# Optimization experiments

Measured on AMD Instinct MI355X. Metric: run time of the kernel, lower is better.

## Reference

```python
import jax, jax.numpy as jnp
import numpy as np

N = 100000      # num nodes
E = 500000      # num edges
IN_DIM = 128
OUT_DIM = 128
H = 8           # n_heads
DK = OUT_DIM // H  # 16


def setup_inputs() -> dict:
    key = jax.random.key(0)
    ks = jax.random.split(key, 16)
    s = 1.0 / np.sqrt(IN_DIM)
    inp = {
        "x": jax.random.normal(ks[0], (N, IN_DIM), dtype=jnp.float32),
        "edge_index": jax.random.randint(ks[1], (2, E), 0, N, dtype=jnp.int64),
        # per-type linear layers (num_types=1)
        "Wk": jax.random.uniform(ks[2], (OUT_DIM, IN_DIM), jnp.float32, -s, s),
        "bk": jnp.zeros((OUT_DIM,), jnp.float32),
        "Wq": jax.random.uniform(ks[3], (OUT_DIM, IN_DIM), jnp.float32, -s, s),
        "bq": jnp.zeros((OUT_DIM,), jnp.float32),
        "Wv": jax.random.uniform(ks[4], (OUT_DIM, IN_DIM), jnp.float32, -s, s),
        "bv": jnp.zeros((OUT_DIM,), jnp.float32),
        "Wa": jax.random.uniform(ks[5], (OUT_DIM, OUT_DIM), jnp.float32, -s, s),
        "ba": jnp.zeros((OUT_DIM,), jnp.float32),
        # per-relation params (num_relations=1), xavier-uniform for d_k x d_k mats
        "R_att": jax.random.uniform(ks[6], (H, DK, DK), jnp.float32, -np.sqrt(6.0 / (2 * DK)), np.sqrt(6.0 / (2 * DK))),
        "R_msg": jax.random.uniform(ks[7], (H, DK, DK), jnp.float32, -np.sqrt(6.0 / (2 * DK)), np.sqrt(6.0 / (2 * DK))),
        "R_pri": jnp.ones((H,), jnp.float32),
        "skip": jnp.ones((), jnp.float32),
    }
    return inp


def reference(x, edge_index, Wk, bk, Wq, bq, Wv, bv, Wa, ba, R_att, R_msg, R_pri, skip):
    sqrt_dk = jnp.asarray(np.sqrt(DK), x.dtype)
    # per-node projections -> [N, H, DK]
    k = (x @ Wk.T + bk).reshape(N, H, DK)
    q = (x @ Wq.T + bq).reshape(N, H, DK)
    v = (x @ Wv.T + bv).reshape(N, H, DK)
    src, dst = edge_index[0], edge_index[1]
    # edge gather: [E, H, DK]
    ke = jnp.einsum('ehd,hdf->ehf', k[src], R_att)
    ve = jnp.einsum('ehd,hdf->ehf', v[src], R_msg)
    qe = q[dst]
    # attention scores [E, H]; softmax over the edge axis (as in the original)
    att = jnp.sum(qe * ke, axis=-1) * R_pri / sqrt_dk
    att = jax.nn.softmax(att, axis=0)
    # weighted sum over all edges -> [H, DK] -> [OUT_DIM]
    out = jnp.einsum('eh,ehf->hf', att, ve).reshape(-1)
    out = Wa @ out + ba  # a_linear on the pooled vector
    alpha = jax.nn.sigmoid(skip)
    # broadcast skip mix against node inputs -> [N, OUT_DIM]
    return out * alpha + x * (1.0 - alpha)
```

## Files before the change

kernel.cpp:

```cpp
#include <hip/hip_runtime.h>
#include <hip/hip_bf16.h>

#define NN 100000
#define EE 500000
#define NB2 256
#define EGRID 2048

typedef __attribute__((ext_vector_type(8))) __bf16 bf16x8;
typedef __attribute__((ext_vector_type(4))) float f32x4;
typedef __attribute__((ext_vector_type(2))) float f32x2;

static const long long OFF_KQ8  = 0;
static const long long OFF_VB   = 6400000;
static const long long OFF_WGT  = 12800000;
static const long long OFF_PART = 13600000;
static const long long OFF_OUTV = 13634816;
static const long long OFF_CNT  = 13634944;
static const long long OFF_WF   = 13635008;
static const long long OFF_BALL = 13659584;

__device__ inline unsigned short f2bf(float f) {
    unsigned int u = __float_as_uint(f);
    unsigned int r = (u + 0x7FFFu + ((u >> 16) & 1u)) >> 16;
    return (unsigned short)r;
}
__device__ inline unsigned int pack2bf(float a, float b) {
    return (unsigned int)f2bf(a) | ((unsigned int)f2bf(b) << 16);
}
#define LOF(u) __uint_as_float((u) << 16)
#define HIF(u) __uint_as_float((u) & 0xffff0000u)

#if __has_builtin(__builtin_amdgcn_cvt_pk_fp8_f32) && __has_builtin(__builtin_amdgcn_cvt_pk_f32_fp8)
#define HW_FP8 1
#endif

__device__ inline unsigned char enc_fp8(float f) {
#ifdef HW_FP8
    int p = __builtin_amdgcn_cvt_pk_fp8_f32(f, f, 0, false);
    return (unsigned char)(p & 0xff);
#else
    unsigned int u = __float_as_uint(f);
    unsigned int s = (u >> 24) & 0x80u;
    unsigned int a = u & 0x7fffffffu;
    if (a >= 0x43e80000u) return (unsigned char)(s | 0x7e);
    if (a < 0x3c800000u) {
        float av = __uint_as_float(a);
        unsigned int m = (unsigned int)rintf(av * 512.0f);
        return (unsigned char)(s | m);
    }
    unsigned int base = a - 0x3c000000u;
    unsigned int r = (base + 0x7ffffu + ((base >> 20) & 1u)) >> 20;
    return (unsigned char)(s | r);
#endif
}

#ifndef HW_FP8
__device__ inline float dec1_fp8(unsigned int b) {
    unsigned int s = (b & 0x80u) << 24;
    unsigned int em = b & 0x7fu;
    float v;
    if (em >= 8u) v = __uint_as_float(s | ((em + 960u) << 20));
    else {
        v = (float)em * 0.001953125f;
        v = __uint_as_float(__float_as_uint(v) | s);
    }
    return v;
}
#endif

__device__ inline float dot4_fp8(unsigned int ka, unsigned int qa, float d) {
#ifdef HW_FP8
    f32x2 k0 = __builtin_amdgcn_cvt_pk_f32_fp8((int)ka, false);
    f32x2 k1 = __builtin_amdgcn_cvt_pk_f32_fp8((int)ka, true);
    f32x2 q0 = __builtin_amdgcn_cvt_pk_f32_fp8((int)qa, false);
    f32x2 q1 = __builtin_amdgcn_cvt_pk_f32_fp8((int)qa, true);
    d = fmaf(k0.x, q0.x, d); d = fmaf(k0.y, q0.y, d);
    d = fmaf(k1.x, q1.x, d); d = fmaf(k1.y, q1.y, d);
    return d;
#else
    #pragma unroll
    for (int i = 0; i < 4; ++i)
        d = fmaf(dec1_fp8((ka >> (8*i)) & 0xff), dec1_fp8((qa >> (8*i)) & 0xff), d);
    return d;
#endif
}

__global__ void prep(const float* __restrict__ Wk, const float* __restrict__ bk,
                     const float* __restrict__ Wq, const float* __restrict__ bq,
                     const float* __restrict__ Wv, const float* __restrict__ bv,
                     const float* __restrict__ R_att,
                     unsigned short* __restrict__ Wf, float* __restrict__ ball,
                     float* __restrict__ Wgt, unsigned int* __restrict__ counter) {
    int j = blockIdx.x;
    int c = threadIdx.x;
    float w;
    if (j < 128) {
        w = Wk[j * 128 + c];
        if (c == 0) ball[j] = bk[j];
    } else if (j < 256) {
        int h = (j - 128) >> 4, d = (j - 128) & 15;
        const float* Rrow = R_att + h * 256 + d * 16;
        float s = 0.f;
        #pragma unroll
        for (int f = 0; f < 16; ++f)
            s = fmaf(Rrow[f], Wq[(h * 16 + f) * 128 + c], s);
        w = s;
        if (c == 0) {
            float sb = 0.f;
            for (int f = 0; f < 16; ++f)
                sb = fmaf(Rrow[f], bq[h * 16 + f], sb);
            ball[j] = sb;
        }
    } else {
        w = Wv[(j - 256) * 128 + c];
        if (c == 0) ball[j] = bv[j - 256];
    }
    int g = j >> 7, wc = (j >> 6) & 1, n = (j >> 4) & 3, lr = j & 15;
    int kk = c >> 5, lk = (c >> 3) & 3, i = c & 7;
    int idx = ((((g * 2 + wc) * 4 + n) * 4 + kk) * 64 + lk * 16 + lr) * 8 + i;
    Wf[idx] = f2bf(w);
    for (int z = j * 128 + c; z < 200000; z += 384 * 128)
        ((float4*)Wgt)[z] = make_float4(0.f, 0.f, 0.f, 0.f);
    if (j == 0 && c == 0) *counter = 0u;
}

__global__ __launch_bounds__(256) void proj_mfma(const float* __restrict__ x,
                                                 const unsigned short* __restrict__ Wf,
                                                 const float* __restrict__ ball,
                                                 unsigned char* __restrict__ kq8,
                                                 unsigned char* __restrict__ vb) {
    __shared__ __align__(16) char cs[16384];
    int tid = threadIdx.x;
    int lane = tid & 63, wv = tid >> 6, wr = wv >> 1, wc = wv & 1;
    int lrow = lane & 15, lk = lane >> 4;
    long long row0 = (long long)blockIdx.x * 64;
    int g = blockIdx.y;
    int col0 = g * 128;

    const float* xr[2];
    #pragma unroll
    for (int m = 0; m < 2; ++m) {
        long long gr = row0 + wr * 32 + m * 16 + lrow;
        if (gr >= NN) gr = NN - 1;
        xr[m] = x + gr * 128;
    }
    const unsigned short* bfb = Wf + (size_t)((g * 2 + wc) * 16) * 512 + lane * 8;

    f32x4 acc[2][4];
    #pragma unroll
    for (int m = 0; m < 2; ++m)
        #pragma unroll
        for (int n = 0; n < 4; ++n)
            acc[m][n] = f32x4{0.f, 0.f, 0.f, 0.f};

    #pragma unroll
    for (int kk = 0; kk < 4; ++kk) {
        bf16x8 a[2], b[4];
        #pragma unroll
        for (int m = 0; m < 2; ++m) {
            const float4* p = (const float4*)(xr[m] + (kk * 4 + lk) * 8);
            float4 u0 = p[0], u1 = p[1];
            union { uint4 u; bf16x8 v; } cv;
            cv.u.x = pack2bf(u0.x, u0.y); cv.u.y = pack2bf(u0.z, u0.w);
            cv.u.z = pack2bf(u1.x, u1.y); cv.u.w = pack2bf(u1.z, u1.w);
            a[m] = cv.v;
        }
        #pragma unroll
        for (int n = 0; n < 4; ++n)
            b[n] = *(const bf16x8*)(bfb + (size_t)(n * 4 + kk) * 512);
        #pragma unroll
        for (int m = 0; m < 2; ++m)
            #pragma unroll
            for (int n = 0; n < 4; ++n)
                acc[m][n] = __builtin_amdgcn_mfma_f32_16x16x32_bf16(a[m], b[n], acc[m][n], 0, 0, 0);
    }

    float bias[4];
    #pragma unroll
    for (int n = 0; n < 4; ++n) bias[n] = ball[col0 + wc * 64 + n * 16 + lrow];

    if (g < 2) {
        unsigned char* C = (unsigned char*)cs;
        #pragma unroll
        for (int m = 0; m < 2; ++m) {
            int rb = wr * 32 + m * 16 + lk * 4;
            #pragma unroll
            for (int n = 0; n < 4; ++n) {
                int cb = wc * 64 + n * 16 + lrow;
                #pragma unroll
                for (int r = 0; r < 4; ++r)
                    C[(rb + r) * 128 + cb] = enc_fp8(acc[m][n][r] + bias[n]);
            }
        }
        __syncthreads();
        #pragma unroll
        for (int it = 0; it < 2; ++it) {
            int c = tid + it * 256;
            int r = c >> 3, sl = c & 7;
            long long gr = row0 + r;
            if (gr < NN)
                *(uint4*)(kq8 + gr * 256 + col0 + sl * 16) = *(const uint4*)(C + r * 128 + sl * 16);
        }
    } else {
        unsigned short* C = (unsigned short*)cs;
        #pragma unroll
        for (int m = 0; m < 2; ++m) {
            int rb = wr * 32 + m * 16 + lk * 4;
            #pragma unroll
            for (int n = 0; n < 4; ++n) {
                int cb = wc * 64 + n * 16 + lrow;
                #pragma unroll
                for (int r = 0; r < 4; ++r)
                    C[(rb + r) * 128 + cb] = f2bf(acc[m][n][r] + bias[n]);
            }
        }
        __syncthreads();
        #pragma unroll
        for (int it = 0; it < 4; ++it) {
            int c = tid + it * 256;
            int r = c >> 4, sl = c & 15;
            long long gr = row0 + r;
            if (gr < NN)
                *(uint4*)(vb + gr * 256 + sl * 16) = *(const uint4*)((const char*)C + r * 256 + sl * 16);
        }
    }
}

__global__ __launch_bounds__(256) void edge_score(const int* __restrict__ ei,
                                                  const unsigned char* __restrict__ kq8,
                                                  const float* __restrict__ R_pri,
                                                  float* __restrict__ Wgt) {
    __shared__ unsigned int pr[256];
    int tid = threadIdx.x;
    const unsigned int* wrd = (const unsigned int*)ei;
    pr[tid] = wrd[2 * tid + 1];
    __syncthreads();
    for (int st = 128; st > 0; st >>= 1) {
        if (tid < st) pr[tid] |= pr[tid + st];
        __syncthreads();
    }
    bool is64 = (pr[0] == 0u);
    int h = tid & 7, es = tid >> 3;
    float rp = R_pri[h] * 0.25f;
    for (int base = blockIdx.x * 32; base < EE; base += EGRID * 32) {
        int e = base + es;
        if (e >= EE) continue;
        int sn, dn;
        if (is64) { sn = ei[2 * e]; dn = ei[2 * (EE + e)]; }
        else      { sn = ei[e];     dn = ei[EE + e]; }
        uint4 kw = *(const uint4*)(kq8 + (size_t)sn * 256 + h * 16);
        uint4 qw = *(const uint4*)(kq8 + (size_t)dn * 256 + 128 + h * 16);
        float d = 0.f;
        d = dot4_fp8(kw.x, qw.x, d); d = dot4_fp8(kw.y, qw.y, d);
        d = dot4_fp8(kw.z, qw.z, d); d = dot4_fp8(kw.w, qw.w, d);
        float w = __expf(d * rp);
        atomicAdd(&Wgt[(size_t)sn * 8 + h], w);
    }
}

__global__ __launch_bounds__(256) void pool_fin(const float* __restrict__ Wgt,
                                                const unsigned char* __restrict__ vb,
                                                float* __restrict__ partial,
                                                unsigned int* __restrict__ counter,
                                                const float* __restrict__ R_msg,
                                                const float* __restrict__ Wa,
                                                const float* __restrict__ ba,
                                                const float* __restrict__ skip,
                                                float* __restrict__ outv) {
    __shared__ float red[256][2];
    __shared__ float redz[256];
    int tid = threadIdx.x;
    int wv = tid >> 6, lane = tid & 63;
    int h = lane >> 3, dp = lane & 7;
    float ax = 0.f, ay = 0.f, zacc = 0.f;
    for (int n = blockIdx.x * 4 + wv; n < NN; n += NB2 * 4) {
        unsigned int vvp = *(const unsigned int*)(vb + (size_t)n * 256 + lane * 4);
        float w = Wgt[(size_t)n * 8 + h];
        ax = fmaf(w, LOF(vvp), ax);
        ay = fmaf(w, HIF(vvp), ay);
        if (dp == 0) zacc += w;
    }
    red[tid][0] = ax; red[tid][1] = ay;
    redz[tid] = (dp == 0) ? zacc : 0.f;
    __syncthreads();
    if (tid < 64) {
        float s0 = red[tid][0] + red[tid+64][0] + red[tid+128][0] + red[tid+192][0];
        float s1 = red[tid][1] + red[tid+64][1] + red[tid+128][1] + red[tid+192][1];
        partial[blockIdx.x * 136 + tid * 2]     = s0;
        partial[blockIdx.x * 136 + tid * 2 + 1] = s1;
        if ((tid & 7) == 0) {
            float z = redz[tid] + redz[tid+64] + redz[tid+128] + redz[tid+192];
            partial[blockIdx.x * 136 + 128 + (tid >> 3)] = z;
        }
    }
    __threadfence();
    __shared__ int amLast;
    if (tid == 0) amLast = (atomicAdd(counter, 1u) == NB2 - 1) ? 1 : 0;
    __syncthreads();
    if (!amLast) return;
    __threadfence();

    __shared__ float poolZ[136];
    for (int c = tid; c < 136; c += 256) {
        float s = 0.f;
        for (int b = 0; b < NB2; ++b) s += partial[b * 136 + c];
        poolZ[c] = s;
    }
    __syncthreads();
    __shared__ float pn[128];
    if (tid < 128) pn[tid] = poolZ[tid] / poolZ[128 + (tid >> 4)];
    __syncthreads();
    __shared__ float msg[128];
    if (tid < 128) {
        int hh = tid >> 4, f = tid & 15;
        float s = 0.f;
        #pragma unroll
        for (int d2 = 0; d2 < 16; ++d2)
            s = fmaf(pn[hh * 16 + d2], R_msg[hh * 256 + d2 * 16 + f], s);
        msg[tid] = s;
    }
    __syncthreads();
    if (tid < 128) {
        float s = ba[tid];
        for (int j = 0; j < 128; ++j) s = fmaf(Wa[tid * 128 + j], msg[j], s);
        float alpha = 1.f / (1.f + __expf(-skip[0]));
        outv[tid] = s * alpha;
    }
}

__global__ __launch_bounds__(256) void broadcast_out(const float* __restrict__ x,
                                                     const float* __restrict__ outv,
                                                     const float* __restrict__ skip,
                                                     float* __restrict__ out) {
    float alpha = 1.f / (1.f + __expf(-skip[0]));
    float beta = 1.f - alpha;
    const int total4 = NN * 128 / 4;
    for (int i = blockIdx.x * blockDim.x + threadIdx.x; i < total4;
         i += gridDim.x * blockDim.x) {
        float4 xv = ((const float4*)x)[i];
        int c4 = i & 31;
        float4 ov = ((const float4*)outv)[c4];
        float4 r;
        r.x = ov.x + beta * xv.x;
        r.y = ov.y + beta * xv.y;
        r.z = ov.z + beta * xv.z;
        r.w = ov.w + beta * xv.w;
        ((float4*)out)[i] = r;
    }
}

extern "C" void kernel_launch(void* const* d_in, const int* in_sizes, int n_in,
                              void* d_out, int out_size, void* d_ws, size_t ws_size,
                              hipStream_t stream) {
    const float* x      = (const float*)d_in[0];
    const int*   ei     = (const int*)d_in[1];
    const float* Wk     = (const float*)d_in[2];
    const float* bk     = (const float*)d_in[3];
    const float* Wq     = (const float*)d_in[4];
    const float* bq     = (const float*)d_in[5];
    const float* Wv     = (const float*)d_in[6];
    const float* bv     = (const float*)d_in[7];
    const float* Wa     = (const float*)d_in[8];
    const float* ba     = (const float*)d_in[9];
    const float* R_att  = (const float*)d_in[10];
    const float* R_msg  = (const float*)d_in[11];
    const float* R_pri  = (const float*)d_in[12];
    const float* skip   = (const float*)d_in[13];
    float* out = (float*)d_out;
    float* ws  = (float*)d_ws;

    unsigned char* kq8 = (unsigned char*)(ws + OFF_KQ8);
    unsigned char* vbp = (unsigned char*)(ws + OFF_VB);
    float* Wgt   = ws + OFF_WGT;
    float* part  = ws + OFF_PART;
    float* outv  = ws + OFF_OUTV;
    unsigned int* counter = (unsigned int*)(ws + OFF_CNT);
    unsigned short* Wf = (unsigned short*)(ws + OFF_WF);
    float* ball  = ws + OFF_BALL;

    prep<<<384, 128, 0, stream>>>(Wk, bk, Wq, bq, Wv, bv, R_att, Wf, ball, Wgt, counter);
    dim3 gg((NN + 63) / 64, 3);
    proj_mfma<<<gg, 256, 0, stream>>>(x, Wf, ball, kq8, vbp);
    edge_score<<<EGRID, 256, 0, stream>>>(ei, kq8, R_pri, Wgt);
    pool_fin<<<NB2, 256, 0, stream>>>(Wgt, vbp, part, counter, R_msg, Wa, ba, skip, outv);
    broadcast_out<<<2048, 256, 0, stream>>>(x, outv, skip, out);
}
```

Baseline: 261.9 us.

## Map one edge per thread and reduce pooled sums with atomics

The edge scoring kernel now gives each thread a whole edge, loading all eight heads' K and Q vectors at once and issuing eight atomics, instead of a grid-stride loop with one head per thread. The pooling kernel runs on more blocks, reads 16 bytes per lane, reduces with warp shuffles, and accumulates into a global pooled buffer with atomics. This removes the last block's serial pass over the per-block partials. The intent is more memory-level parallelism and a shorter tail, at the cost of more atomic traffic and wider, less coalesced per-thread gathers.

Result: slower. 459.8 us (+75.5%).

```diff
diff --git a/kernel.cpp b/kernel.cpp
--- a/kernel.cpp
+++ b/kernel.cpp
@@ -3,8 +3,8 @@
 
 #define NN 100000
 #define EE 500000
-#define NB2 256
-#define EGRID 2048
+#define NPB 1024
+#define EB  ((EE + 255) / 256)
 
 typedef __attribute__((ext_vector_type(8))) __bf16 bf16x8;
 typedef __attribute__((ext_vector_type(4))) float f32x4;
@@ -13,7 +13,7 @@
 static const long long OFF_KQ8  = 0;
 static const long long OFF_VB   = 6400000;
 static const long long OFF_WGT  = 12800000;
-static const long long OFF_PART = 13600000;
+static const long long OFF_PZ   = 13600000;
 static const long long OFF_OUTV = 13634816;
 static const long long OFF_CNT  = 13634944;
 static const long long OFF_WF   = 13635008;
@@ -90,7 +90,8 @@
                      const float* __restrict__ Wv, const float* __restrict__ bv,
                      const float* __restrict__ R_att,
                      unsigned short* __restrict__ Wf, float* __restrict__ ball,
-                     float* __restrict__ Wgt, unsigned int* __restrict__ counter) {
+                     float* __restrict__ Wgt, float* __restrict__ pooledZ,
+                     unsigned int* __restrict__ counter) {
     int j = blockIdx.x;
     int c = threadIdx.x;
     float w;
@@ -122,6 +123,7 @@
     for (int z = j * 128 + c; z < 200000; z += 384 * 128)
         ((float4*)Wgt)[z] = make_float4(0.f, 0.f, 0.f, 0.f);
     if (j == 0 && c == 0) *counter = 0u;
+    if (j == 1 && c < 136) pooledZ[c] = 0.f;
 }
 
 __global__ __launch_bounds__(256) void proj_mfma(const float* __restrict__ x,
@@ -226,86 +228,99 @@
     }
 }
 
-__global__ __launch_bounds__(256) void edge_score(const int* __restrict__ ei,
-                                                  const unsigned char* __restrict__ kq8,
-                                                  const float* __restrict__ R_pri,
-                                                  float* __restrict__ Wgt) {
+__global__ __launch_bounds__(256) void edge_all(const int* __restrict__ ei,
+                                                const unsigned char* __restrict__ kq8,
+                                                const float* __restrict__ R_pri,
+                                                float* __restrict__ Wgt) {
     __shared__ unsigned int pr[256];
+    __shared__ float rps[8];
     int tid = threadIdx.x;
-    const unsigned int* wrd = (const unsigned int*)ei;
-    pr[tid] = wrd[2 * tid + 1];
+    pr[tid] = ((const unsigned int*)ei)[2 * tid + 1];
+    if (tid < 8) rps[tid] = R_pri[tid] * 0.25f;
     __syncthreads();
     for (int st = 128; st > 0; st >>= 1) {
         if (tid < st) pr[tid] |= pr[tid + st];
         __syncthreads();
     }
     bool is64 = (pr[0] == 0u);
-    int h = tid & 7, es = tid >> 3;
-    float rp = R_pri[h] * 0.25f;
-    for (int base = blockIdx.x * 32; base < EE; base += EGRID * 32) {
-        int e = base + es;
-        if (e >= EE) continue;
-        int sn, dn;
-        if (is64) { sn = ei[2 * e]; dn = ei[2 * (EE + e)]; }
-        else      { sn = ei[e];     dn = ei[EE + e]; }
-        uint4 kw = *(const uint4*)(kq8 + (size_t)sn * 256 + h * 16);
-        uint4 qw = *(const uint4*)(kq8 + (size_t)dn * 256 + 128 + h * 16);
+    int e = blockIdx.x * 256 + tid;
+    if (e >= EE) return;
+    int sn, dn;
+    if (is64) { sn = ei[2 * e]; dn = ei[2 * (EE + e)]; }
+    else      { sn = ei[e];     dn = ei[EE + e]; }
+    const uint4* kp = (const uint4*)(kq8 + (size_t)sn * 256);
+    const uint4* qp = (const uint4*)(kq8 + (size_t)dn * 256 + 128);
+    uint4 kw[8], qw[8];
+    #pragma unroll
+    for (int h = 0; h < 8; ++h) { kw[h] = kp[h]; qw[h] = qp[h]; }
+    #pragma unroll
+    for (int h = 0; h < 8; ++h) {
         float d = 0.f;
-        d = dot4_fp8(kw.x, qw.x, d); d = dot4_fp8(kw.y, qw.y, d);
-        d = dot4_fp8(kw.z, qw.z, d); d = dot4_fp8(kw.w, qw.w, d);
-        float w = __expf(d * rp);
+        d = dot4_fp8(kw[h].x, qw[h].x, d); d = dot4_fp8(kw[h].y, qw[h].y, d);
+        d = dot4_fp8(kw[h].z, qw[h].z, d); d = dot4_fp8(kw[h].w, qw[h].w, d);
+        float w = __expf(d * rps[h]);
         atomicAdd(&Wgt[(size_t)sn * 8 + h], w);
     }
 }
 
 __global__ __launch_bounds__(256) void pool_fin(const float* __restrict__ Wgt,
                                                 const unsigned char* __restrict__ vb,
-                                                float* __restrict__ partial,
+                                                float* __restrict__ pooledZ,
                                                 unsigned int* __restrict__ counter,
                                                 const float* __restrict__ R_msg,
                                                 const float* __restrict__ Wa,
                                                 const float* __restrict__ ba,
                                                 const float* __restrict__ skip,
                                                 float* __restrict__ outv) {
-    __shared__ float red[256][2];
-    __shared__ float redz[256];
     int tid = threadIdx.x;
-    int wv = tid >> 6, lane = tid & 63;
-    int h = lane >> 3, dp = lane & 7;
-    float ax = 0.f, ay = 0.f, zacc = 0.f;
-    for (int n = blockIdx.x * 4 + wv; n < NN; n += NB2 * 4) {
-        unsigned int vvp = *(const unsigned int*)(vb + (size_t)n * 256 + lane * 4);
-        float w = Wgt[(size_t)n * 8 + h];
-        ax = fmaf(w, LOF(vvp), ax);
-        ay = fmaf(w, HIF(vvp), ay);
-        if (dp == 0) zacc += w;
-    }
-    red[tid][0] = ax; red[tid][1] = ay;
-    redz[tid] = (dp == 0) ? zacc : 0.f;
-    __syncthreads();
-    if (tid < 64) {
-        float s0 = red[tid][0] + red[tid+64][0] + red[tid+128][0] + red[tid+192][0];
-        float s1 = red[tid][1] + red[tid+64][1] + red[tid+128][1] + red[tid+192][1];
-        partial[blockIdx.x * 136 + tid * 2]     = s0;
-        partial[blockIdx.x * 136 + tid * 2 + 1] = s1;
-        if ((tid & 7) == 0) {
-            float z = redz[tid] + redz[tid+64] + redz[tid+128] + redz[tid+192];
-            partial[blockIdx.x * 136 + 128 + (tid >> 3)] = z;
-        }
+    int wv = tid >> 6, l = tid & 63;
+    int grp = l & 15, sub = l >> 4;
+    int h = grp >> 1;
+    float acc[8] = {0.f, 0.f, 0.f, 0.f, 0.f, 0.f, 0.f, 0.f};
+    float zacc = 0.f;
+    for (int n0 = blockIdx.x * 16 + wv * 4; n0 < NN; n0 += NPB * 16) {
+        int node = n0 + sub;
+        if (node < NN) {
+            uint4 vv = *(const uint4*)(vb + (size_t)node * 256 + grp * 16);
+            float w = Wgt[(size_t)node * 8 + h];
+            acc[0] = fmaf(w, LOF(vv.x), acc[0]); acc[1] = fmaf(w, HIF(vv.x), acc[1]);
+            acc[2] = fmaf(w, LOF(vv.y), acc[2]); acc[3] = fmaf(w, HIF(vv.y), acc[3]);
+            acc[4] = fmaf(w, LOF(vv.z), acc[4]); acc[5] = fmaf(w, HIF(vv.z), acc[5]);
+            acc[6] = fmaf(w, LOF(vv.w), acc[6]); acc[7] = fmaf(w, HIF(vv.w), acc[7]);
+            if ((grp & 1) == 0) zacc += w;
+        }
+    }
+    #pragma unroll
+    for (int off = 16; off <= 32; off <<= 1) {
+        #pragma unroll
+        for (int j = 0; j < 8; ++j) acc[j] += __shfl_xor(acc[j], off);
+        zacc += __shfl_xor(zacc, off);
+    }
+    __shared__ float sm[4][16][8];
+    __shared__ float smz[4][8];
+    if (l < 16) {
+        #pragma unroll
+        for (int j = 0; j < 8; ++j) sm[wv][l][j] = acc[j];
+        if ((l & 1) == 0) smz[wv][l >> 1] = zacc;
+    }
+    __syncthreads();
+    if (tid < 128) {
+        int gg = tid >> 3, j = tid & 7;
+        float s = sm[0][gg][j] + sm[1][gg][j] + sm[2][gg][j] + sm[3][gg][j];
+        atomicAdd(&pooledZ[tid], s);
+    }
+    if (tid < 8) {
+        float z = smz[0][tid] + smz[1][tid] + smz[2][tid] + smz[3][tid];
+        atomicAdd(&pooledZ[128 + tid], z);
     }
     __threadfence();
     __shared__ int amLast;
-    if (tid == 0) amLast = (atomicAdd(counter, 1u) == NB2 - 1) ? 1 : 0;
+    if (tid == 0) amLast = (atomicAdd(counter, 1u) == NPB - 1) ? 1 : 0;
     __syncthreads();
     if (!amLast) return;
-    __threadfence();
 
     __shared__ float poolZ[136];
-    for (int c = tid; c < 136; c += 256) {
-        float s = 0.f;
-        for (int b = 0; b < NB2; ++b) s += partial[b * 136 + c];
-        poolZ[c] = s;
-    }
+    if (tid < 136) poolZ[tid] = atomicAdd(&pooledZ[tid], 0.f);
     __syncthreads();
     __shared__ float pn[128];
     if (tid < 128) pn[tid] = poolZ[tid] / poolZ[128 + (tid >> 4)];
@@ -372,16 +387,16 @@
     unsigned char* kq8 = (unsigned char*)(ws + OFF_KQ8);
     unsigned char* vbp = (unsigned char*)(ws + OFF_VB);
     float* Wgt   = ws + OFF_WGT;
-    float* part  = ws + OFF_PART;
+    float* pz    = ws + OFF_PZ;
     float* outv  = ws + OFF_OUTV;
     unsigned int* counter = (unsigned int*)(ws + OFF_CNT);
     unsigned short* Wf = (unsigned short*)(ws + OFF_WF);
     float* ball  = ws + OFF_BALL;
 
-    prep<<<384, 128, 0, stream>>>(Wk, bk, Wq, bq, Wv, bv, R_att, Wf, ball, Wgt, counter);
+    prep<<<384, 128, 0, stream>>>(Wk, bk, Wq, bq, Wv, bv, R_att, Wf, ball, Wgt, pz, counter);
     dim3 gg((NN + 63) / 64, 3);
     proj_mfma<<<gg, 256, 0, stream>>>(x, Wf, ball, kq8, vbp);
-    edge_score<<<EGRID, 256, 0, stream>>>(ei, kq8, R_pri, Wgt);
-    pool_fin<<<NB2, 256, 0, stream>>>(Wgt, vbp, part, counter, R_msg, Wa, ba, skip, outv);
+    edge_all<<<EB, 256, 0, stream>>>(ei, kq8, R_pri, Wgt);
+    pool_fin<<<NPB, 256, 0, stream>>>(Wgt, vbp, pz, counter, R_msg, Wa, ba, skip, outv);
     broadcast_out<<<2048, 256, 0, stream>>>(x, outv, skip, out);
 }
```
